# Performance work log

Hardware: AMD Instinct MI355X
Metric: run time of the kernel (lower is better)

The kernel has to match this reference:

```python
import jax, jax.numpy as jnp
import numpy as np

DIM = 1024
N_HEADS = 16
HEAD_DIM = DIM // N_HEADS
LN_EPS = 1e-5


def layer_norm(x, gamma, beta, eps=LN_EPS):
    mu = jnp.mean(x, axis=-1, keepdims=True)
    var = jnp.var(x, axis=-1, keepdims=True)
    return (x - mu) * jax.lax.rsqrt(var + eps) * gamma + beta


def setup_inputs() -> dict:
    key = jax.random.key(0)
    ks = jax.random.split(key, 12)
    B, Nq, Nc, D = 2, 1024, 4096, DIM
    s = 1.0 / np.sqrt(D)  # torch Linear default init scale (uniform bound)
    inp = {
        "query": jax.random.normal(ks[0], (B, Nq, D), jnp.float32),
        "context": jax.random.normal(ks[1], (B, Nc, D), jnp.float32),
        "wq": jax.random.uniform(ks[2], (D, D), jnp.float32, -s, s),
        "bq": jax.random.uniform(ks[3], (D,), jnp.float32, -s, s),
        "wk": jax.random.uniform(ks[4], (D, D), jnp.float32, -s, s),
        "bk": jax.random.uniform(ks[5], (D,), jnp.float32, -s, s),
        "wv": jax.random.uniform(ks[6], (D, D), jnp.float32, -s, s),
        "bv": jax.random.uniform(ks[7], (D,), jnp.float32, -s, s),
        "wo": jax.random.uniform(ks[8], (D, D), jnp.float32, -s, s),
        "bo": jax.random.uniform(ks[9], (D,), jnp.float32, -s, s),
        "g_q": jnp.ones((D,), jnp.float32),
        "b_q": jnp.zeros((D,), jnp.float32),
        "g_kv": jnp.ones((D,), jnp.float32),
        "b_kv": jnp.zeros((D,), jnp.float32),
    }
    return inp


def reference(query, context, wq, bq, wk, bk, wv, bv, wo, bo, g_q, b_q, g_kv, b_kv):
    B, Nq, D = query.shape
    Nc = context.shape[1]
    H, Hd = N_HEADS, HEAD_DIM

    qn = layer_norm(query, g_q, b_q)        # [B,Nq,D]
    cn = layer_norm(context, g_kv, b_kv)    # [B,Nc,D]

    # torch Linear: y = x @ W.T + b; weights here stored as [out,in]
    Q = (jnp.einsum('bnd,ed->bne', qn, wq) + bq).reshape(B, Nq, H, Hd)
    K = (jnp.einsum('bnd,ed->bne', cn, wk) + bk).reshape(B, Nc, H, Hd)
    V = (jnp.einsum('bnd,ed->bne', cn, wv) + bv).reshape(B, Nc, H, Hd)

    scale = 1.0 / np.sqrt(Hd)
    scores = jnp.einsum('bqhd,bkhd->bhqk', Q, K) * scale  # [B,H,Nq,Nc]
    attn = jax.nn.softmax(scores, axis=-1)
    out = jnp.einsum('bhqk,bkhd->bqhd', attn, V).reshape(B, Nq, D)

    return qn + (jnp.einsum('bnd,ed->bne', out, wo) + bo)
```

## Files before the change

### kernel.cpp

```cpp
#include <hip/hip_runtime.h>

typedef unsigned short u16;
typedef __attribute__((ext_vector_type(8))) __bf16 bf16x8;
typedef __attribute__((ext_vector_type(4))) float f32x4;

struct alignas(8) U16x4 { u16 x, y, z, w; };

__device__ __forceinline__ u16 f2bf(float f) {
    union { float f; unsigned u; } v; v.f = f;
    unsigned r = v.u + 0x7fffu + ((v.u >> 16) & 1u);
    return (u16)(r >> 16);
}

__device__ __forceinline__ unsigned cvt_pk_bf16(float lo, float hi) {
    unsigned r;
    asm("v_cvt_pk_bf16_f32 %0, %1, %2" : "=v"(r) : "v"(lo), "v"(hi));
    return r;
}

__device__ __forceinline__ float fexp2(float x) {
    float r;
    asm("v_exp_f32 %0, %1" : "=v"(r) : "v"(x));
    return r;
}

__device__ __forceinline__ void gload_lds16(const void* g, void* l) {
    __builtin_amdgcn_global_load_lds(
        (__attribute__((address_space(1))) void*)g,
        (__attribute__((address_space(3))) void*)l, 16, 0, 0);
}

__global__ __launch_bounds__(256)
void ln_fused(const float* __restrict__ x, const float* __restrict__ g,
              const float* __restrict__ be, float* __restrict__ y32,
              u16* __restrict__ y16)
{
    const int wid = threadIdx.x >> 6, lane = threadIdx.x & 63;
    const size_t row = (size_t)blockIdx.x * 4 + wid;
    const float4* xr = (const float4*)(x + row * 1024);
    float4 v[4];
    float s = 0.f, ss = 0.f;
#pragma unroll
    for (int i = 0; i < 4; ++i) {
        v[i] = xr[i * 64 + lane];
        s  += (v[i].x + v[i].y) + (v[i].z + v[i].w);
        ss += (v[i].x * v[i].x + v[i].y * v[i].y) + (v[i].z * v[i].z + v[i].w * v[i].w);
    }
#pragma unroll
    for (int o = 32; o; o >>= 1) { s += __shfl_xor(s, o, 64); ss += __shfl_xor(ss, o, 64); }
    const float mu = s * (1.f / 1024.f);
    const float rstd = rsqrtf(ss * (1.f / 1024.f) - mu * mu + 1e-5f);
#pragma unroll
    for (int i = 0; i < 4; ++i) {
        float4 gv = ((const float4*)g)[i * 64 + lane];
        float4 bv = ((const float4*)be)[i * 64 + lane];
        float4 o;
        o.x = (v[i].x - mu) * rstd * gv.x + bv.x;
        o.y = (v[i].y - mu) * rstd * gv.y + bv.y;
        o.z = (v[i].z - mu) * rstd * gv.z + bv.z;
        o.w = (v[i].w - mu) * rstd * gv.w + bv.w;
        if (y32) ((float4*)(y32 + row * 1024))[i * 64 + lane] = o;
        U16x4 pk = { f2bf(o.x), f2bf(o.y), f2bf(o.z), f2bf(o.w) };
        ((U16x4*)(y16 + row * 1024))[i * 64 + lane] = pk;
    }
}

__global__ __launch_bounds__(256)
void wconv4(const float4* __restrict__ a, const float4* __restrict__ b,
            const float4* __restrict__ c, const float4* __restrict__ d,
            U16x4* __restrict__ oa, U16x4* __restrict__ ob,
            U16x4* __restrict__ oc, U16x4* __restrict__ od)
{
    const int i = blockIdx.x * 256 + threadIdx.x;
    float4 v;
    v = a[i]; oa[i] = { f2bf(v.x), f2bf(v.y), f2bf(v.z), f2bf(v.w) };
    v = b[i]; ob[i] = { f2bf(v.x), f2bf(v.y), f2bf(v.z), f2bf(v.w) };
    v = c[i]; oc[i] = { f2bf(v.x), f2bf(v.y), f2bf(v.z), f2bf(v.w) };
    v = d[i]; od[i] = { f2bf(v.x), f2bf(v.y), f2bf(v.z), f2bf(v.w) };
}

template<int MODE>
__global__ __launch_bounds__(256)
void gemm_bt(const u16* __restrict__ A, const u16* __restrict__ W,
             const float* __restrict__ bias, const float* __restrict__ resid,
             void* __restrict__ Cp, int M, int N, int K, float alpha)
{
    constexpr int BK = 64;
    __shared__ __align__(16) u16 sA[128 * BK];
    __shared__ __align__(16) u16 sB[128 * BK];
    const int tid = threadIdx.x, wid = tid >> 6, lane = tid & 63;
    const int lr = lane & 15, lg = lane >> 4;
    const int wr = wid >> 1, wc = wid & 1;
    const int row0 = blockIdx.x * 128, col0 = blockIdx.y * 128;
    const int srow = wid * 8 + (lane >> 3), scol = (lane & 7) * 8;

    const u16* Ag = A + (size_t)(row0 + srow) * K + scol;
    const u16* Wg = W + (size_t)(col0 + srow) * K + scol;

    f32x4 acc[4][4];
#pragma unroll
    for (int m = 0; m < 4; ++m)
#pragma unroll
        for (int n = 0; n < 4; ++n) acc[m][n] = (f32x4){0.f, 0.f, 0.f, 0.f};

    for (int k0 = 0; k0 < K; k0 += BK) {
        __syncthreads();
#pragma unroll
        for (int i = 0; i < 4; ++i)
            gload_lds16(Ag + (size_t)i * 32 * K + k0, (char*)sA + i * 4096 + wid * 1024);
#pragma unroll
        for (int i = 0; i < 4; ++i)
            gload_lds16(Wg + (size_t)i * 32 * K + k0, (char*)sB + i * 4096 + wid * 1024);
        __syncthreads();
#pragma unroll
        for (int kk = 0; kk < 2; ++kk) {
            bf16x8 af[4], bfr[4];
#pragma unroll
            for (int m = 0; m < 4; ++m)
                af[m] = *(const bf16x8*)&sA[(wr * 64 + m * 16 + lr) * BK + kk * 32 + lg * 8];
#pragma unroll
            for (int n = 0; n < 4; ++n)
                bfr[n] = *(const bf16x8*)&sB[(wc * 64 + n * 16 + lr) * BK + kk * 32 + lg * 8];
#pragma unroll
            for (int m = 0; m < 4; ++m)
#pragma unroll
                for (int n = 0; n < 4; ++n)
                    acc[m][n] = __builtin_amdgcn_mfma_f32_16x16x32_bf16(af[m], bfr[n], acc[m][n], 0, 0, 0);
        }
    }

#pragma unroll
    for (int m = 0; m < 4; ++m) {
#pragma unroll
        for (int n = 0; n < 4; ++n) {
            const int r = row0 + wr * 64 + m * 16 + lg * 4;
            const int c = col0 + wc * 64 + n * 16 + lr;
            const float bv = bias[c];
            if constexpr (MODE == 0) {
                u16* C = (u16*)Cp;
#pragma unroll
                for (int j = 0; j < 4; ++j)
                    C[(size_t)(r + j) * N + c] = f2bf((acc[m][n][j] + bv) * alpha);
            } else if constexpr (MODE == 1) {
                float* C = (float*)Cp;
#pragma unroll
                for (int j = 0; j < 4; ++j)
                    C[(size_t)(r + j) * N + c] =
                        (acc[m][n][j] + bv) * alpha + resid[(size_t)(r + j) * N + c];
            } else {
                u16* C = (u16*)Cp;
                const size_t base = ((size_t)(r >> 12) * 1024 + c) * 4096 + (r & 4095);
                U16x4 pk = { f2bf((acc[m][n][0] + bv) * alpha),
                             f2bf((acc[m][n][1] + bv) * alpha),
                             f2bf((acc[m][n][2] + bv) * alpha),
                             f2bf((acc[m][n][3] + bv) * alpha) };
                *(U16x4*)&C[base] = pk;
            }
        }
    }
}

__global__ __launch_bounds__(512, 4)
void attn_fwd(const u16* __restrict__ Q, const u16* __restrict__ Kg,
              const u16* __restrict__ Vt, u16* __restrict__ O)
{
    constexpr int D = 1024, CSTR = 19;
    __shared__ __align__(16) char smem[81920];

    const int tid = threadIdx.x, wid = tid >> 6, lane = tid & 63;
    const int grp = wid >> 2, w = wid & 3;
    const int lr = lane & 15, lg = lane >> 4;
    const int rs = lr & 7;
    const int pkey = (lr & 7) << 4;

    const int fid = blockIdx.x;
    const int wk = (fid & 7) * 64 + (fid >> 3);
    const int qblk = wk & 15, h = (wk >> 4) & 15, b = wk >> 8;
    const int q0 = qblk * 64 + w * 16;

    const u16* Qrow = Q + (size_t)(b * 1024 + q0 + lr) * D + h * 64;
    const bf16x8 qf0 = *(const bf16x8*)(Qrow + lg * 8);
    const bf16x8 qf1 = *(const bf16x8*)(Qrow + 32 + lg * 8);

    const int srow = w * 8 + (lane >> 3);
    const int scol = ((lane & 7) ^ (srow & 7)) * 8;
    const u16* kp = Kg + (size_t)(b * 4096 + grp * 2048 + srow) * D + h * 64 + scol;
    const u16* vp = Vt + ((size_t)(b * 16 + h) * 64 + srow) * 4096 + grp * 2048 + scol;

    char* sProw = smem + 65536 + wid * 2048 + lr * 128;

    f32x4 po[4];
#pragma unroll
    for (int df = 0; df < 4; ++df) po[df] = (f32x4){0.f, 0.f, 0.f, 0.f};
    float m = -INFINITY, l = 0.f;

    {
        char* kd = smem + grp * 8192 + w * 1024;
        char* vd = smem + 32768 + grp * 8192 + w * 1024;
        gload_lds16(kp,                      kd);
        gload_lds16(kp + (size_t)32 * D,     kd + 4096);
        gload_lds16(vp,                      vd);
        gload_lds16(vp + (size_t)32 * 4096,  vd + 4096);
        kp += (size_t)64 * D; vp += 64;
    }
    asm volatile("s_waitcnt vmcnt(0)" ::: "memory");
    asm volatile("s_barrier" ::: "memory");

    for (int t = 0; t < 32; ++t) {
        const int cur = t & 1;
        if (t < 31) {
            char* kd = smem + (cur ^ 1) * 16384 + grp * 8192 + w * 1024;
            char* vd = smem + 32768 + (cur ^ 1) * 16384 + grp * 8192 + w * 1024;
            gload_lds16(kp,                      kd);
            gload_lds16(kp + (size_t)32 * D,     kd + 4096);
            gload_lds16(vp,                      vd);
            gload_lds16(vp + (size_t)32 * 4096,  vd + 4096);
            kp += (size_t)64 * D; vp += 64;
        }

        const u16* kb = (const u16*)(smem + cur * 16384 + grp * 8192);
        const u16* vb = (const u16*)(smem + 32768 + cur * 16384 + grp * 8192);

        f32x4 s4[4];
#pragma unroll
        for (int f = 0; f < 4; ++f) {
            const int r = f * 16 + lr;
            bf16x8 k0v = *(const bf16x8*)&kb[r * 64 + (lg ^ rs) * 8];
            bf16x8 k1v = *(const bf16x8*)&kb[r * 64 + ((lg + 4) ^ rs) * 8];
            f32x4 z = (f32x4){0.f, 0.f, 0.f, 0.f};
            z = __builtin_amdgcn_mfma_f32_16x16x32_bf16(k0v, qf0, z, 0, 0, 0);
            s4[f] = __builtin_amdgcn_mfma_f32_16x16x32_bf16(k1v, qf1, z, 0, 0, 0);
        }

        float pmax = fmaxf(fmaxf(fmaxf(s4[0][0], s4[0][1]), fmaxf(s4[0][2], s4[0][3])),
                     fmaxf(fmaxf(fmaxf(s4[1][0], s4[1][1]), fmaxf(s4[1][2], s4[1][3])),
                     fmaxf(fmaxf(fmaxf(s4[2][0], s4[2][1]), fmaxf(s4[2][2], s4[2][3])),
                           fmaxf(fmaxf(s4[3][0], s4[3][1]), fmaxf(s4[3][2], s4[3][3])))));
        if (!__all(pmax <= m)) {
            float tmax = fmaxf(pmax, __shfl_xor(pmax, 16, 64));
            tmax = fmaxf(tmax, __shfl_xor(tmax, 32, 64));
            const float mn = fmaxf(m, tmax);
            const float corr = fexp2(m - mn);
            l *= corr;
#pragma unroll
            for (int df = 0; df < 4; ++df) po[df] *= corr;
            m = mn;
        }
        float lsum = 0.f;
        uint2 pk[4];
#pragma unroll
        for (int f = 0; f < 4; ++f) {
            float p0 = fexp2(s4[f][0] - m);
            float p1 = fexp2(s4[f][1] - m);
            float p2 = fexp2(s4[f][2] - m);
            float p3 = fexp2(s4[f][3] - m);
            lsum += (p0 + p1) + (p2 + p3);
            pk[f].x = cvt_pk_bf16(p0, p1);
            pk[f].y = cvt_pk_bf16(p2, p3);
        }
        l += lsum;

#pragma unroll
        for (int f = 0; f < 4; ++f)
            *(uint2*)(sProw + ((f * 32 + lg * 8) ^ pkey)) = pk[f];

#pragma unroll
        for (int c = 0; c < 2; ++c) {
            bf16x8 pf = *(const bf16x8*)(sProw + ((c * 64 + lg * 16) ^ pkey));
#pragma unroll
            for (int df = 0; df < 4; ++df) {
                const int r = df * 16 + lr;
                bf16x8 vf = *(const bf16x8*)&vb[r * 64 + ((c * 4 + lg) ^ rs) * 8];
                po[df] = __builtin_amdgcn_mfma_f32_16x16x32_bf16(vf, pf, po[df], 0, 0, 0);
            }
        }

        asm volatile("s_waitcnt vmcnt(0)" ::: "memory");
        asm volatile("s_barrier" ::: "memory");
    }

    l += __shfl_xor(l, 16, 64);
    l += __shfl_xor(l, 32, 64);

    float* cb = (float*)smem;
    if (grp == 1) {
        float* dst = cb + (size_t)(w * 64 + lane) * CSTR;
        dst[0] = m; dst[1] = l;
#pragma unroll
        for (int df = 0; df < 4; ++df)
#pragma unroll
            for (int j = 0; j < 4; ++j) dst[2 + df * 4 + j] = po[df][j];
    }
    __syncthreads();
    if (grp == 0) {
        const float* src = cb + (size_t)(w * 64 + lane) * CSTR;
        const float m1 = src[0], l1 = src[1];
        const float M = fmaxf(m, m1);
        const float c0 = fexp2(m - M), c1 = fexp2(m1 - M);
        const float rl = 1.f / (l * c0 + l1 * c1);
        u16* Orow = O + (size_t)(b * 1024 + q0 + lr) * D + h * 64;
#pragma unroll
        for (int df = 0; df < 4; ++df) {
            U16x4 opk = { f2bf((po[df][0] * c0 + src[2 + df * 4 + 0] * c1) * rl),
                          f2bf((po[df][1] * c0 + src[2 + df * 4 + 1] * c1) * rl),
                          f2bf((po[df][2] * c0 + src[2 + df * 4 + 2] * c1) * rl),
                          f2bf((po[df][3] * c0 + src[2 + df * 4 + 3] * c1) * rl) };
            *(U16x4*)&Orow[df * 16 + lg * 4] = opk;
        }
    }
}

extern "C" void kernel_launch(void* const* d_in, const int* in_sizes, int n_in,
                              void* d_out, int out_size, void* d_ws, size_t ws_size,
                              hipStream_t stream)
{
    const float* query   = (const float*)d_in[0];
    const float* context = (const float*)d_in[1];
    const float* wq = (const float*)d_in[2];
    const float* bq = (const float*)d_in[3];
    const float* wk = (const float*)d_in[4];
    const float* bk = (const float*)d_in[5];
    const float* wv = (const float*)d_in[6];
    const float* bv = (const float*)d_in[7];
    const float* wo = (const float*)d_in[8];
    const float* bo = (const float*)d_in[9];
    const float* g_q  = (const float*)d_in[10];
    const float* b_q  = (const float*)d_in[11];
    const float* g_kv = (const float*)d_in[12];
    const float* b_kv = (const float*)d_in[13];

    char* p = (char*)d_ws;
    auto alloc = [&](size_t bytes) { char* r = p; p += (bytes + 255) & ~(size_t)255; return r; };
    u16*   wqb  = (u16*)alloc(1024 * 1024 * 2);
    u16*   wkb  = (u16*)alloc(1024 * 1024 * 2);
    u16*   wvb  = (u16*)alloc(1024 * 1024 * 2);
    u16*   wob  = (u16*)alloc(1024 * 1024 * 2);
    float* qn32 = (float*)alloc((size_t)2048 * 1024 * 4);
    u16*   qnb  = (u16*)alloc((size_t)2048 * 1024 * 2);
    u16*   cnb  = (u16*)alloc((size_t)8192 * 1024 * 2);
    u16*   Qb   = (u16*)alloc((size_t)2048 * 1024 * 2);
    u16*   Kb   = (u16*)alloc((size_t)8192 * 1024 * 2);
    u16*   Vtb  = (u16*)alloc((size_t)8192 * 1024 * 2);
    u16*   AOb  = (u16*)alloc((size_t)2048 * 1024 * 2);

    wconv4<<<1024, 256, 0, stream>>>((const float4*)wq, (const float4*)wk,
                                     (const float4*)wv, (const float4*)wo,
                                     (U16x4*)wqb, (U16x4*)wkb, (U16x4*)wvb, (U16x4*)wob);
    ln_fused<<<512, 256, 0, stream>>>(query, g_q, b_q, qn32, qnb);
    ln_fused<<<2048, 256, 0, stream>>>(context, g_kv, b_kv, nullptr, cnb);

    gemm_bt<0><<<dim3(16, 8), 256, 0, stream>>>(qnb, wqb, bq, nullptr, Qb, 2048, 1024, 1024, 0.18033688f);
    gemm_bt<0><<<dim3(64, 8), 256, 0, stream>>>(cnb, wkb, bk, nullptr, Kb, 8192, 1024, 1024, 1.0f);
    gemm_bt<2><<<dim3(64, 8), 256, 0, stream>>>(cnb, wvb, bv, nullptr, Vtb, 8192, 1024, 1024, 1.0f);

    attn_fwd<<<dim3(512), 512, 0, stream>>>(Qb, Kb, Vtb, AOb);

    gemm_bt<1><<<dim3(16, 8), 256, 0, stream>>>(AOb, wob, bo, qn32, d_out, 2048, 1024, 1024, 1.0f);
}
```

Before: 193.7 us.

## Fuse K and V projections into one GEMM and shrink Q/O GEMM tiles

The K and V projection GEMMs become one kernel with 512 threads. It loads each context tile once into LDS and multiplies it against both weight matrices, so the activation matrix is read from global memory once instead of twice. The Q and output projection GEMMs switch to a 64-row tile, which doubles the block count for the small 2048-row problems and should fill the GPU better. In exchange the fused kernel uses more LDS and registers, and the smaller tiles give less reuse of each loaded weight tile.

```diff
diff --git a/kernel.cpp b/kernel.cpp
--- a/kernel.cpp
+++ b/kernel.cpp
@@ -79,34 +79,111 @@
     v = d[i]; od[i] = { f2bf(v.x), f2bf(v.y), f2bf(v.z), f2bf(v.w) };
 }
 
+__global__ __launch_bounds__(512, 4)
+void gemm_kv(const u16* __restrict__ A, const u16* __restrict__ Wk,
+             const u16* __restrict__ Wv, const float* __restrict__ bkp,
+             const float* __restrict__ bvp, u16* __restrict__ Kout,
+             u16* __restrict__ Vt)
+{
+    constexpr int K = 1024, N = 1024, BK = 64;
+    __shared__ __align__(16) u16 sA[128 * BK];
+    __shared__ __align__(16) u16 sK[128 * BK];
+    __shared__ __align__(16) u16 sV[128 * BK];
+    const int tid = threadIdx.x, wid = tid >> 6, lane = tid & 63;
+    const int lr = lane & 15, lg = lane >> 4;
+    const int wr = wid >> 2, wc = wid & 3;
+    const int row0 = blockIdx.x * 128, col0 = blockIdx.y * 128;
+    const int srow = wid * 8 + (lane >> 3), scol = (lane & 7) * 8;
+
+    const u16* Ag = A  + (size_t)(row0 + srow) * K + scol;
+    const u16* Kg = Wk + (size_t)(col0 + srow) * K + scol;
+    const u16* Vg = Wv + (size_t)(col0 + srow) * K + scol;
+
+    f32x4 ka[4][2], va[4][2];
+#pragma unroll
+    for (int m = 0; m < 4; ++m)
+#pragma unroll
+        for (int n = 0; n < 2; ++n) {
+            ka[m][n] = (f32x4){0.f, 0.f, 0.f, 0.f};
+            va[m][n] = (f32x4){0.f, 0.f, 0.f, 0.f};
+        }
+
+    for (int k0 = 0; k0 < K; k0 += BK) {
+        __syncthreads();
+#pragma unroll
+        for (int i = 0; i < 2; ++i) {
+            gload_lds16(Ag + (size_t)i * 64 * K + k0, (char*)sA + i * 8192 + wid * 1024);
+            gload_lds16(Kg + (size_t)i * 64 * K + k0, (char*)sK + i * 8192 + wid * 1024);
+            gload_lds16(Vg + (size_t)i * 64 * K + k0, (char*)sV + i * 8192 + wid * 1024);
+        }
+        __syncthreads();
+#pragma unroll
+        for (int kk = 0; kk < 2; ++kk) {
+            bf16x8 af[4], bk[2], bv[2];
+#pragma unroll
+            for (int m = 0; m < 4; ++m)
+                af[m] = *(const bf16x8*)&sA[(wr * 64 + m * 16 + lr) * BK + kk * 32 + lg * 8];
+#pragma unroll
+            for (int n = 0; n < 2; ++n) {
+                bk[n] = *(const bf16x8*)&sK[(wc * 32 + n * 16 + lr) * BK + kk * 32 + lg * 8];
+                bv[n] = *(const bf16x8*)&sV[(wc * 32 + n * 16 + lr) * BK + kk * 32 + lg * 8];
+            }
+#pragma unroll
+            for (int m = 0; m < 4; ++m)
+#pragma unroll
+                for (int n = 0; n < 2; ++n) {
+                    ka[m][n] = __builtin_amdgcn_mfma_f32_16x16x32_bf16(af[m], bk[n], ka[m][n], 0, 0, 0);
+                    va[m][n] = __builtin_amdgcn_mfma_f32_16x16x32_bf16(af[m], bv[n], va[m][n], 0, 0, 0);
+                }
+        }
+    }
+
+#pragma unroll
+    for (int m = 0; m < 4; ++m) {
+#pragma unroll
+        for (int n = 0; n < 2; ++n) {
+            const int r = row0 + wr * 64 + m * 16 + lg * 4;
+            const int c = col0 + wc * 32 + n * 16 + lr;
+            const float kb = bkp[c], vb = bvp[c];
+#pragma unroll
+            for (int j = 0; j < 4; ++j)
+                Kout[(size_t)(r + j) * N + c] = f2bf(ka[m][n][j] + kb);
+            const size_t base = ((size_t)(r >> 12) * 1024 + c) * 4096 + (r & 4095);
+            U16x4 pk = { f2bf(va[m][n][0] + vb), f2bf(va[m][n][1] + vb),
+                         f2bf(va[m][n][2] + vb), f2bf(va[m][n][3] + vb) };
+            *(U16x4*)&Vt[base] = pk;
+        }
+    }
+}
+
 template<int MODE>
 __global__ __launch_bounds__(256)
-void gemm_bt(const u16* __restrict__ A, const u16* __restrict__ W,
-             const float* __restrict__ bias, const float* __restrict__ resid,
-             void* __restrict__ Cp, int M, int N, int K, float alpha)
+void gemm_bt64(const u16* __restrict__ A, const u16* __restrict__ W,
+               const float* __restrict__ bias, const float* __restrict__ resid,
+               void* __restrict__ Cp, int M, int N, int K, float alpha)
 {
     constexpr int BK = 64;
-    __shared__ __align__(16) u16 sA[128 * BK];
+    __shared__ __align__(16) u16 sA[64 * BK];
     __shared__ __align__(16) u16 sB[128 * BK];
     const int tid = threadIdx.x, wid = tid >> 6, lane = tid & 63;
     const int lr = lane & 15, lg = lane >> 4;
     const int wr = wid >> 1, wc = wid & 1;
-    const int row0 = blockIdx.x * 128, col0 = blockIdx.y * 128;
+    const int row0 = blockIdx.x * 64, col0 = blockIdx.y * 128;
     const int srow = wid * 8 + (lane >> 3), scol = (lane & 7) * 8;
 
     const u16* Ag = A + (size_t)(row0 + srow) * K + scol;
     const u16* Wg = W + (size_t)(col0 + srow) * K + scol;
 
-    f32x4 acc[4][4];
-#pragma unroll
-    for (int m = 0; m < 4; ++m)
+    f32x4 acc[2][4];
+#pragma unroll
+    for (int m = 0; m < 2; ++m)
 #pragma unroll
         for (int n = 0; n < 4; ++n) acc[m][n] = (f32x4){0.f, 0.f, 0.f, 0.f};
 
     for (int k0 = 0; k0 < K; k0 += BK) {
         __syncthreads();
 #pragma unroll
-        for (int i = 0; i < 4; ++i)
+        for (int i = 0; i < 2; ++i)
             gload_lds16(Ag + (size_t)i * 32 * K + k0, (char*)sA + i * 4096 + wid * 1024);
 #pragma unroll
         for (int i = 0; i < 4; ++i)
@@ -114,15 +191,15 @@
         __syncthreads();
 #pragma unroll
         for (int kk = 0; kk < 2; ++kk) {
-            bf16x8 af[4], bfr[4];
-#pragma unroll
-            for (int m = 0; m < 4; ++m)
-                af[m] = *(const bf16x8*)&sA[(wr * 64 + m * 16 + lr) * BK + kk * 32 + lg * 8];
+            bf16x8 af[2], bfr[4];
+#pragma unroll
+            for (int m = 0; m < 2; ++m)
+                af[m] = *(const bf16x8*)&sA[(wr * 32 + m * 16 + lr) * BK + kk * 32 + lg * 8];
 #pragma unroll
             for (int n = 0; n < 4; ++n)
                 bfr[n] = *(const bf16x8*)&sB[(wc * 64 + n * 16 + lr) * BK + kk * 32 + lg * 8];
 #pragma unroll
-            for (int m = 0; m < 4; ++m)
+            for (int m = 0; m < 2; ++m)
 #pragma unroll
                 for (int n = 0; n < 4; ++n)
                     acc[m][n] = __builtin_amdgcn_mfma_f32_16x16x32_bf16(af[m], bfr[n], acc[m][n], 0, 0, 0);
@@ -130,10 +207,10 @@
     }
 
 #pragma unroll
-    for (int m = 0; m < 4; ++m) {
+    for (int m = 0; m < 2; ++m) {
 #pragma unroll
         for (int n = 0; n < 4; ++n) {
-            const int r = row0 + wr * 64 + m * 16 + lg * 4;
+            const int r = row0 + wr * 32 + m * 16 + lg * 4;
             const int c = col0 + wc * 64 + n * 16 + lr;
             const float bv = bias[c];
             if constexpr (MODE == 0) {
@@ -141,20 +218,12 @@
 #pragma unroll
                 for (int j = 0; j < 4; ++j)
                     C[(size_t)(r + j) * N + c] = f2bf((acc[m][n][j] + bv) * alpha);
-            } else if constexpr (MODE == 1) {
+            } else {
                 float* C = (float*)Cp;
 #pragma unroll
                 for (int j = 0; j < 4; ++j)
                     C[(size_t)(r + j) * N + c] =
                         (acc[m][n][j] + bv) * alpha + resid[(size_t)(r + j) * N + c];
-            } else {
-                u16* C = (u16*)Cp;
-                const size_t base = ((size_t)(r >> 12) * 1024 + c) * 4096 + (r & 4095);
-                U16x4 pk = { f2bf((acc[m][n][0] + bv) * alpha),
-                             f2bf((acc[m][n][1] + bv) * alpha),
-                             f2bf((acc[m][n][2] + bv) * alpha),
-                             f2bf((acc[m][n][3] + bv) * alpha) };
-                *(U16x4*)&C[base] = pk;
             }
         }
     }
@@ -349,11 +418,10 @@
     ln_fused<<<512, 256, 0, stream>>>(query, g_q, b_q, qn32, qnb);
     ln_fused<<<2048, 256, 0, stream>>>(context, g_kv, b_kv, nullptr, cnb);
 
-    gemm_bt<0><<<dim3(16, 8), 256, 0, stream>>>(qnb, wqb, bq, nullptr, Qb, 2048, 1024, 1024, 0.18033688f);
-    gemm_bt<0><<<dim3(64, 8), 256, 0, stream>>>(cnb, wkb, bk, nullptr, Kb, 8192, 1024, 1024, 1.0f);
-    gemm_bt<2><<<dim3(64, 8), 256, 0, stream>>>(cnb, wvb, bv, nullptr, Vtb, 8192, 1024, 1024, 1.0f);
+    gemm_bt64<0><<<dim3(32, 8), 256, 0, stream>>>(qnb, wqb, bq, nullptr, Qb, 2048, 1024, 1024, 0.18033688f);
+    gemm_kv<<<dim3(64, 8), 512, 0, stream>>>(cnb, wkb, wvb, bk, bv, Kb, Vtb);
 
     attn_fwd<<<dim3(512), 512, 0, stream>>>(Qb, Kb, Vtb, AOb);
 
-    gemm_bt<1><<<dim3(16, 8), 256, 0, stream>>>(AOb, wob, bo, qn32, d_out, 2048, 1024, 1024, 1.0f);
-}
+    gemm_bt64<1><<<dim3(32, 8), 256, 0, stream>>>(AOb, wob, bo, qn32, d_out, 2048, 1024, 1024, 1.0f);
+}
```

New measurement: 169.3 us. 1.14x faster.
